# Kernel optimization log

Measured on AMD Instinct MI355X. Metric: run time of the kernel, lower is better.

The kernel has to match this reference:

```python
import jax, jax.numpy as jnp
import numpy as np

E_LAMBDA = 1e-4


def _conv1d(x, w, b=None, pad=0):
    # x: (C, L) unbatched, w: (O, I, K)
    y = jax.lax.conv_general_dilated(
        x[None], w, window_strides=(1,), padding=[(pad, pad)],
        dimension_numbers=("NCH", "OIH", "NCH"))[0]
    if b is not None:
        y = y + b[:, None]
    return y


def _avg_pool2(x):
    # kernel 2 stride 2 along last axis; x: (C, L) -> (C, L//2)
    C, L = x.shape
    return x.reshape(C, L // 2, 2).mean(axis=-1)


def _simam(x):
    # x: (C, L); torch version runs on (1, C, L) so stats are global
    n = x.shape[0] * x.shape[1] - 1
    d = (x - x.mean()) ** 2
    y = d / (4.0 * (d.sum() / n + E_LAMBDA)) + 0.5
    return x + x * jax.nn.sigmoid(y)


def setup_inputs() -> dict:
    key = jax.random.key(0)
    ks = jax.random.split(key, 6)
    C, L = 2048, 4096  # L must equal 2*C for Tiss broadcast to be valid
    inp = jax.random.normal(ks[0], (C, L), dtype=jnp.float32)
    insum = jax.random.normal(ks[1], (C, L), dtype=jnp.float32)
    conv1_w = jax.random.normal(ks[2], (C, C, 3), dtype=jnp.float32) * (1.0 / np.sqrt(3 * C))
    fc_w = jax.random.normal(ks[3], (C, C, 1), dtype=jnp.float32) * (1.0 / np.sqrt(C))
    fc_b = jax.random.normal(ks[4], (C,), dtype=jnp.float32) * 0.01
    mix_w = jnp.array([-0.8], dtype=jnp.float32)
    return {"input": inp, "insum": insum, "conv1_w": conv1_w,
            "fc_w": fc_w, "fc_b": fc_b, "mix_w": mix_w}


def reference(input, insum, conv1_w, fc_w, fc_b, mix_w):
    x = _avg_pool2(input)        # (C, L/2)
    x_mfcc = _avg_pool2(insum)   # (C, L/2)

    input_new = _simam(input)
    insum_new = _simam(insum)

    x1 = _conv1d(x, conv1_w, pad=1)          # (C, L/2)
    x_mfcc1 = _conv1d(x_mfcc, conv1_w, pad=1)
    x2 = _conv1d(x, fc_w, fc_b, pad=0).T      # (L/2, C)
    x_mfcc2 = _conv1d(x_mfcc1, fc_w, fc_b, pad=0).T  # (L/2, C)

    out1 = jax.nn.sigmoid((x1 @ x_mfcc2).sum(axis=1))          # (C,)
    out2 = jax.nn.sigmoid((x_mfcc1.T @ x2.T).sum(axis=1))      # (L/2,) == (C,)

    mf = jax.nn.sigmoid(mix_w)                                  # (1,)
    out = out1 * mf + out2 * (1.0 - mf)                         # (C,)

    out = jax.nn.sigmoid(_conv1d(out[:, None], conv1_w, pad=1))  # (C, 1)

    input_insum = input_new * 0.6 + insum_new * 0.4             # (C, L)
    return input_insum * out
```

## Files before the change

### kernel.cpp

```cpp
#include <hip/hip_runtime.h>
#include <math.h>

#define C  2048
#define L  4096
#define L2 2048
#define CW3 6144

constexpr size_t OFF_RS_A = 0;
constexpr size_t OFF_RQ_A = 2048;
constexpr size_t OFF_RS_B = 4096;
constexpr size_t OFF_RQ_B = 6144;
constexpr size_t OFF_SCAL = 8192;
constexpr size_t OFF_V    = 8208;
constexpr size_t OFF_O2   = 10256;
constexpr size_t OFF_S    = 12304;
constexpr size_t OFF_U    = 14352;
constexpr size_t OFF_MIX  = 20496;

constexpr size_t CWP_OFF = 0;
constexpr size_t GP_OFF  = 65536;
constexpr size_t HP_OFF  = 458752;

__device__ __forceinline__ float wredf(float v) {
#pragma unroll
  for (int o = 32; o; o >>= 1) v += __shfl_down(v, o, 64);
  return v;
}
__device__ __forceinline__ double wredd(double v) {
#pragma unroll
  for (int o = 32; o; o >>= 1) v += __shfl_down(v, o, 64);
  return v;
}
__device__ __forceinline__ float sigm(float x) { return 1.f / (1.f + expf(-x)); }
__device__ __forceinline__ float simam1(float x, float m, float cf) {
  float d = x - m;
  float y = d * d * cf + 0.5f;
  return x * (1.f + 1.f / (1.f + expf(-y)));
}

__global__ void k1(const float* __restrict__ A, const float* __restrict__ B,
                   const float* __restrict__ fc_w, float* __restrict__ ws,
                   float* __restrict__ scr) {
  int u = blockIdx.x, tid = threadIdx.x;
  if (u < 2048) {
    __shared__ float sm[16];
    const float4* pa = (const float4*)(A + (size_t)u * L);
    const float4* pb = (const float4*)(B + (size_t)u * L);
    float sa = 0.f, qa = 0.f, sb = 0.f, qb = 0.f;
#pragma unroll
    for (int i = tid; i < L / 4; i += 256) {
      float4 va = pa[i], vb = pb[i];
      sa += (va.x + va.y) + (va.z + va.w);
      qa += (va.x * va.x + va.y * va.y) + (va.z * va.z + va.w * va.w);
      sb += (vb.x + vb.y) + (vb.z + vb.w);
      qb += (vb.x * vb.x + vb.y * vb.y) + (vb.z * vb.z + vb.w * vb.w);
    }
    sa = wredf(sa); qa = wredf(qa); sb = wredf(sb); qb = wredf(qb);
    int lane = tid & 63, wv = tid >> 6;
    if (!lane) { sm[wv] = sa; sm[4 + wv] = qa; sm[8 + wv] = sb; sm[12 + wv] = qb; }
    __syncthreads();
    if (!tid) {
      ws[OFF_RS_A + u] = sm[0] + sm[1] + sm[2] + sm[3];
      ws[OFF_RQ_A + u] = sm[4] + sm[5] + sm[6] + sm[7];
      ws[OFF_RS_B + u] = sm[8] + sm[9] + sm[10] + sm[11];
      ws[OFF_RQ_B + u] = sm[12] + sm[13] + sm[14] + sm[15];
    }
  } else {
    int cb = u - 2048;
    int rg = cb >> 3;
    int col = (cb & 7) * 256 + tid;
    const float* p = fc_w + (size_t)rg * 64 * C + col;
    float acc = 0.f;
#pragma unroll 8
    for (int k = 0; k < 64; ++k) acc += p[(size_t)k * C];
    scr[CWP_OFF + (size_t)rg * 2048 + col] = acc;
  }
}

__global__ void k2(const float* __restrict__ fc_w, const float* __restrict__ fc_b,
                   float* __restrict__ ws) {
  int u = blockIdx.x, tid = threadIdx.x;
  int lane = tid & 63, wv = tid >> 6;
  if (u < 512) {
    __shared__ float sl[16];
    int r0 = u * 4;
    const float4* rx = (const float4*)(ws + OFF_RS_A);
    const float4* w4 = (const float4*)fc_w;
    float a0 = 0.f, a1 = 0.f, a2 = 0.f, a3 = 0.f;
#pragma unroll
    for (int i = tid; i < C / 4; i += 256) {
      float4 r = rx[i];
      float4 w0 = w4[(size_t)(r0 + 0) * 512 + i];
      float4 w1 = w4[(size_t)(r0 + 1) * 512 + i];
      float4 w2 = w4[(size_t)(r0 + 2) * 512 + i];
      float4 w3 = w4[(size_t)(r0 + 3) * 512 + i];
      a0 += w0.x * r.x + w0.y * r.y + w0.z * r.z + w0.w * r.w;
      a1 += w1.x * r.x + w1.y * r.y + w1.z * r.z + w1.w * r.w;
      a2 += w2.x * r.x + w2.y * r.y + w2.z * r.z + w2.w * r.w;
      a3 += w3.x * r.x + w3.y * r.y + w3.z * r.z + w3.w * r.w;
    }
    a0 = wredf(a0); a1 = wredf(a1); a2 = wredf(a2); a3 = wredf(a3);
    if (!lane) { sl[wv] = a0; sl[4 + wv] = a1; sl[8 + wv] = a2; sl[12 + wv] = a3; }
    __syncthreads();
    if (tid < 4) {
      float s_ = sl[tid * 4 + 0] + sl[tid * 4 + 1] + sl[tid * 4 + 2] + sl[tid * 4 + 3];
      ws[OFF_S + r0 + tid] = 0.5f * s_ + (float)L2 * fc_b[r0 + tid];
    }
  } else {
    __shared__ double sd[5];
    const float* arr = ws + (wv == 0 ? OFF_RS_A : wv == 1 ? OFF_RQ_A
                                                          : wv == 2 ? OFF_RS_B : OFF_RQ_B);
    double acc = 0.0, accb = 0.0;
    for (int i = lane; i < 2048; i += 64) {
      acc += (double)arr[i];
      if (wv == 0) accb += (double)fc_b[i];
    }
    acc = wredd(acc);
    if (wv == 0) accb = wredd(accb);
    if (!lane) { sd[wv] = acc; if (wv == 0) sd[4] = accb; }
    __syncthreads();
    if (!tid) {
      const double N = (double)C * (double)L, n = N - 1.0;
      double dA = sd[1] - sd[0] * sd[0] / N;
      double dB = sd[3] - sd[2] * sd[2] / N;
      float* sc = ws + OFF_SCAL;
      sc[0] = (float)(sd[0] / N);
      sc[1] = (float)(1.0 / (4.0 * (dA / n + 1e-4)));
      sc[2] = (float)(sd[2] / N);
      sc[3] = (float)(1.0 / (4.0 * (dB / n + 1e-4)));
      sc[4] = (float)sd[4];
    }
  }
}

__global__ void k3(const float* __restrict__ conv1_w, const float* __restrict__ ws,
                   float* __restrict__ scr) {
  __shared__ float lcw[32], ls[32];
  int u = blockIdx.x, tid = threadIdx.x;
  int rg = u / 6, cc = u % 6;
  int i0 = rg * 32;
  int col4 = cc * 256 + tid;
  if (tid < 32) {
    float a = 0.f;
#pragma unroll 8
    for (int g = 0; g < 32; ++g) a += scr[CWP_OFF + (size_t)g * 2048 + i0 + tid];
    lcw[tid] = a;
    ls[tid] = ws[OFF_S + i0 + tid];
  }
  __syncthreads();
  const float4* cv = (const float4*)conv1_w;
  float4 g4 = {0.f, 0.f, 0.f, 0.f}, h4 = {0.f, 0.f, 0.f, 0.f};
#pragma unroll 8
  for (int k = 0; k < 32; ++k) {
    float4 w = cv[(size_t)(i0 + k) * 1536 + col4];
    float cwv = lcw[k], sv = ls[k];
    g4.x += cwv * w.x; g4.y += cwv * w.y; g4.z += cwv * w.z; g4.w += cwv * w.w;
    h4.x += sv * w.x;  h4.y += sv * w.y;  h4.z += sv * w.z;  h4.w += sv * w.w;
  }
  ((float4*)(scr + GP_OFF + (size_t)rg * 6144))[col4] = g4;
  ((float4*)(scr + HP_OFF + (size_t)rg * 6144))[col4] = h4;
}

__global__ void k4(const float* __restrict__ insum, const float* __restrict__ scr,
                   float* __restrict__ ws) {
  __shared__ float gs[96], hs[96];
  int u = blockIdx.x, tid = threadIdx.x;
  int kb = u & 7, cg = u >> 3;
  int c0 = cg * 32;
  int k = kb * 256 + tid;
  if (tid < 192) {
    int t = (tid < 96) ? tid : tid - 96;
    const float* base = scr + ((tid < 96) ? GP_OFF : HP_OFF) + (size_t)c0 * 3 + t;
    float a = 0.f;
#pragma unroll 8
    for (int g = 0; g < 64; ++g) a += base[(size_t)g * 6144];
    if (tid < 96) gs[t] = a; else hs[t] = a;
  }
  __syncthreads();
  float accv = 0.f, acco = 0.f;
#pragma unroll 8
  for (int c = 0; c < 32; ++c) {
    const float* row = insum + (size_t)(c0 + c) * L;
    float2 fm = *(const float2*)(row + 2 * k);
    float xc = 0.5f * (fm.x + fm.y);
    float xl = 0.f, xr = 0.f;
    if (k > 0)      { float2 f = *(const float2*)(row + 2 * k - 2); xl = 0.5f * (f.x + f.y); }
    if (k < L2 - 1) { float2 f = *(const float2*)(row + 2 * k + 2); xr = 0.5f * (f.x + f.y); }
    accv += gs[c * 3] * xl + gs[c * 3 + 1] * xc + gs[c * 3 + 2] * xr;
    acco += hs[c * 3] * xl + hs[c * 3 + 1] * xc + hs[c * 3 + 2] * xr;
  }
  atomicAdd(ws + OFF_V + k, accv);
  atomicAdd(ws + OFF_O2 + k, acco);
}

__global__ void k5(const float* __restrict__ input, float* __restrict__ ws) {
  __shared__ float vsh[2050];
  __shared__ float s12[12];
  int u = blockIdx.x, tid = threadIdx.x;
  float sb = (ws + OFF_SCAL)[4];
  if (tid == 0) { vsh[0] = 0.f; vsh[2049] = 0.f; }
  for (int j = tid; j < L2; j += 256) vsh[1 + j] = (ws + OFF_V)[j] + sb;
  __syncthreads();
  const float4* prow = (const float4*)(input + (size_t)u * L);
  float a0 = 0.f, a1 = 0.f, a2 = 0.f;
#pragma unroll
  for (int i = tid; i < L / 4; i += 256) {
    float4 f = prow[i];
    float p0 = 0.5f * (f.x + f.y), p1 = 0.5f * (f.z + f.w);
    int j = 2 * i;
    a0 += p0 * vsh[j + 2] + p1 * vsh[j + 3];
    a1 += p0 * vsh[j + 1] + p1 * vsh[j + 2];
    a2 += p0 * vsh[j]     + p1 * vsh[j + 1];
  }
  a0 = wredf(a0); a1 = wredf(a1); a2 = wredf(a2);
  int lane = tid & 63, wv = tid >> 6;
  if (!lane) { s12[wv] = a0; s12[4 + wv] = a1; s12[8 + wv] = a2; }
  __syncthreads();
  if (!tid) {
    (ws + OFF_U)[u * 3 + 0] = s12[0] + s12[1] + s12[2] + s12[3];
    (ws + OFF_U)[u * 3 + 1] = s12[4] + s12[5] + s12[6] + s12[7];
    (ws + OFF_U)[u * 3 + 2] = s12[8] + s12[9] + s12[10] + s12[11];
  }
}

__global__ void k6(const float* __restrict__ conv1_w, const float* __restrict__ mix_w,
                   float* __restrict__ ws) {
  __shared__ float sl[4];
  int u = blockIdx.x, tid = threadIdx.x;
  const float4* w4p = (const float4*)(conv1_w + (size_t)u * CW3);
  const float4* u4 = (const float4*)(ws + OFF_U);
  float acc = 0.f;
#pragma unroll
  for (int m = tid; m < CW3 / 4; m += 256) {
    float4 wv = w4p[m], uv = u4[m];
    acc += wv.x * uv.x + wv.y * uv.y + wv.z * uv.z + wv.w * uv.w;
  }
  acc = wredf(acc);
  int lane = tid & 63, wv = tid >> 6;
  if (!lane) sl[wv] = acc;
  __syncthreads();
  if (!tid) {
    float mfv = sigm(mix_w[0]);
    float o1 = sigm(sl[0] + sl[1] + sl[2] + sl[3]);
    float o2 = sigm((ws + OFF_O2)[u]);
    (ws + OFF_MIX)[u] = o1 * mfv + o2 * (1.f - mfv);
  }
}

__global__ void k7(const float* __restrict__ input, const float* __restrict__ insum,
                   const float* __restrict__ conv1_w, float* __restrict__ out,
                   const float* __restrict__ ws) {
  __shared__ float sl[4];
  __shared__ float shov;
  int u = blockIdx.x, tid = threadIdx.x;
  const float4* w4p = (const float4*)(conv1_w + (size_t)u * CW3);
  const float4* m4 = (const float4*)(ws + OFF_MIX);
  float acc = 0.f;
#pragma unroll
  for (int p = tid; p < 512; p += 256) {
    float4 f0 = w4p[3 * p], f1 = w4p[3 * p + 1], f2 = w4p[3 * p + 2];
    float4 m = m4[p];
    acc += f0.y * m.x + f1.x * m.y + f1.w * m.z + f2.z * m.w;
  }
  acc = wredf(acc);
  int lane = tid & 63, wv = tid >> 6;
  if (!lane) sl[wv] = acc;
  __syncthreads();
  if (!tid) shov = sigm(sl[0] + sl[1] + sl[2] + sl[3]);
  __syncthreads();
  float ovc = shov;
  const float* scal = ws + OFF_SCAL;
  float mA = scal[0], cA = scal[1], mB = scal[2], cB = scal[3];
  size_t base = (size_t)u * L;
  const float4* pa = (const float4*)(input + base);
  const float4* pb = (const float4*)(insum + base);
  float4* po = (float4*)(out + base);
#pragma unroll
  for (int i = tid; i < L / 4; i += 256) {
    float4 a = pa[i], b = pb[i], r;
    r.x = (simam1(a.x, mA, cA) * 0.6f + simam1(b.x, mB, cB) * 0.4f) * ovc;
    r.y = (simam1(a.y, mA, cA) * 0.6f + simam1(b.y, mB, cB) * 0.4f) * ovc;
    r.z = (simam1(a.z, mA, cA) * 0.6f + simam1(b.z, mB, cB) * 0.4f) * ovc;
    r.w = (simam1(a.w, mA, cA) * 0.6f + simam1(b.w, mB, cB) * 0.4f) * ovc;
    po[i] = r;
  }
}

extern "C" void kernel_launch(void* const* d_in, const int* in_sizes, int n_in,
                              void* d_out, int out_size, void* d_ws, size_t ws_size,
                              hipStream_t stream) {
  const float* input   = (const float*)d_in[0];
  const float* insum   = (const float*)d_in[1];
  const float* conv1_w = (const float*)d_in[2];
  const float* fc_w    = (const float*)d_in[3];
  const float* fc_b    = (const float*)d_in[4];
  const float* mix_w   = (const float*)d_in[5];
  float* out = (float*)d_out;
  float* ws  = (float*)d_ws;

  hipMemsetAsync((char*)d_ws + OFF_V * 4, 0, 4096 * 4, stream);

  dim3 b(256);
  k1<<<2304, b, 0, stream>>>(input, insum, fc_w, ws, out);
  k2<<<513, b, 0, stream>>>(fc_w, fc_b, ws);
  k3<<<384, b, 0, stream>>>(conv1_w, ws, out);
  k4<<<512, b, 0, stream>>>(insum, out, ws);
  k5<<<2048, b, 0, stream>>>(input, ws);
  k6<<<2048, b, 0, stream>>>(conv1_w, mix_w, ws);
  k7<<<2048, b, 0, stream>>>(input, insum, conv1_w, out, ws);
}
```

Before: 246.8 us.

## Fuse fc_w GEMV into conv-weight kernel, fold memset into k1, shuffle neighbors in k4

The separate k2 kernel, which computed the fc_w·rowsum GEMV and the global statistics, is merged into k3. Each of k3's 384 blocks now recomputes the 32 fc rows it needs locally, and one extra block handles the global statistics. The hipMemsetAsync of the V/O2 accumulators moves into 16 extra blocks of k1. In k4, left and right pooled neighbors now come from wave shuffles instead of extra global loads. Together these remove two launches and some redundant memory traffic, but k3 now re-reads fc_w rows 6 times (once per column chunk), which adds global traffic.

```diff
diff --git a/kernel.cpp b/kernel.cpp
--- a/kernel.cpp
+++ b/kernel.cpp
@@ -13,9 +13,8 @@
 constexpr size_t OFF_SCAL = 8192;
 constexpr size_t OFF_V    = 8208;
 constexpr size_t OFF_O2   = 10256;
-constexpr size_t OFF_S    = 12304;
-constexpr size_t OFF_U    = 14352;
-constexpr size_t OFF_MIX  = 20496;
+constexpr size_t OFF_U    = 12304;
+constexpr size_t OFF_MIX  = 18448;
 
 constexpr size_t CWP_OFF = 0;
 constexpr size_t GP_OFF  = 65536;
@@ -65,7 +64,7 @@
       ws[OFF_RS_B + u] = sm[8] + sm[9] + sm[10] + sm[11];
       ws[OFF_RQ_B + u] = sm[12] + sm[13] + sm[14] + sm[15];
     }
-  } else {
+  } else if (u < 2304) {
     int cb = u - 2048;
     int rg = cb >> 3;
     int col = (cb & 7) * 256 + tid;
@@ -74,40 +73,57 @@
 #pragma unroll 8
     for (int k = 0; k < 64; ++k) acc += p[(size_t)k * C];
     scr[CWP_OFF + (size_t)rg * 2048 + col] = acc;
-  }
-}
-
-__global__ void k2(const float* __restrict__ fc_w, const float* __restrict__ fc_b,
-                   float* __restrict__ ws) {
-  int u = blockIdx.x, tid = threadIdx.x;
-  int lane = tid & 63, wv = tid >> 6;
-  if (u < 512) {
-    __shared__ float sl[16];
-    int r0 = u * 4;
-    const float4* rx = (const float4*)(ws + OFF_RS_A);
-    const float4* w4 = (const float4*)fc_w;
-    float a0 = 0.f, a1 = 0.f, a2 = 0.f, a3 = 0.f;
-#pragma unroll
-    for (int i = tid; i < C / 4; i += 256) {
-      float4 r = rx[i];
-      float4 w0 = w4[(size_t)(r0 + 0) * 512 + i];
-      float4 w1 = w4[(size_t)(r0 + 1) * 512 + i];
-      float4 w2 = w4[(size_t)(r0 + 2) * 512 + i];
-      float4 w3 = w4[(size_t)(r0 + 3) * 512 + i];
-      a0 += w0.x * r.x + w0.y * r.y + w0.z * r.z + w0.w * r.w;
-      a1 += w1.x * r.x + w1.y * r.y + w1.z * r.z + w1.w * r.w;
-      a2 += w2.x * r.x + w2.y * r.y + w2.z * r.z + w2.w * r.w;
-      a3 += w3.x * r.x + w3.y * r.y + w3.z * r.z + w3.w * r.w;
-    }
-    a0 = wredf(a0); a1 = wredf(a1); a2 = wredf(a2); a3 = wredf(a3);
-    if (!lane) { sl[wv] = a0; sl[4 + wv] = a1; sl[8 + wv] = a2; sl[12 + wv] = a3; }
+  } else {
+    int idx = (u - 2304) * 256 + tid;
+    ws[OFF_V + idx] = 0.f;
+  }
+}
+
+__global__ void k3(const float* __restrict__ conv1_w, const float* __restrict__ fc_w,
+                   const float* __restrict__ fc_b, float* __restrict__ ws,
+                   float* __restrict__ scr) {
+  int u = blockIdx.x, tid = threadIdx.x;
+  if (u < 384) {
+    __shared__ float lcw[32], ls[32];
+    int rg = u / 6, cc = u % 6;
+    int i0 = rg * 32;
+    int col4 = cc * 256 + tid;
+    {
+      int r = tid >> 3, g = tid & 7;
+      const float4* wrow = (const float4*)(fc_w + (size_t)(i0 + r) * C);
+      const float4* rx = (const float4*)(ws + OFF_RS_A);
+      float acc = 0.f;
+#pragma unroll 8
+      for (int j = g; j < C / 4; j += 8) {
+        float4 w = wrow[j], rv = rx[j];
+        acc += w.x * rv.x + w.y * rv.y + w.z * rv.z + w.w * rv.w;
+      }
+      acc += __shfl_xor(acc, 1, 64);
+      acc += __shfl_xor(acc, 2, 64);
+      acc += __shfl_xor(acc, 4, 64);
+      if (g == 0) ls[r] = 0.5f * acc + (float)L2 * fc_b[i0 + r];
+    }
+    if (tid < 32) {
+      float a = 0.f;
+#pragma unroll 8
+      for (int g = 0; g < 32; ++g) a += scr[CWP_OFF + (size_t)g * 2048 + i0 + tid];
+      lcw[tid] = a;
+    }
     __syncthreads();
-    if (tid < 4) {
-      float s_ = sl[tid * 4 + 0] + sl[tid * 4 + 1] + sl[tid * 4 + 2] + sl[tid * 4 + 3];
-      ws[OFF_S + r0 + tid] = 0.5f * s_ + (float)L2 * fc_b[r0 + tid];
-    }
+    const float4* cv = (const float4*)conv1_w;
+    float4 g4 = {0.f, 0.f, 0.f, 0.f}, h4 = {0.f, 0.f, 0.f, 0.f};
+#pragma unroll 8
+    for (int k = 0; k < 32; ++k) {
+      float4 w = cv[(size_t)(i0 + k) * 1536 + col4];
+      float cwv = lcw[k], sv = ls[k];
+      g4.x += cwv * w.x; g4.y += cwv * w.y; g4.z += cwv * w.z; g4.w += cwv * w.w;
+      h4.x += sv * w.x;  h4.y += sv * w.y;  h4.z += sv * w.z;  h4.w += sv * w.w;
+    }
+    ((float4*)(scr + GP_OFF + (size_t)rg * 6144))[col4] = g4;
+    ((float4*)(scr + HP_OFF + (size_t)rg * 6144))[col4] = h4;
   } else {
     __shared__ double sd[5];
+    int lane = tid & 63, wv = tid >> 6;
     const float* arr = ws + (wv == 0 ? OFF_RS_A : wv == 1 ? OFF_RQ_A
                                                           : wv == 2 ? OFF_RS_B : OFF_RQ_B);
     double acc = 0.0, accb = 0.0;
@@ -133,34 +149,6 @@
   }
 }
 
-__global__ void k3(const float* __restrict__ conv1_w, const float* __restrict__ ws,
-                   float* __restrict__ scr) {
-  __shared__ float lcw[32], ls[32];
-  int u = blockIdx.x, tid = threadIdx.x;
-  int rg = u / 6, cc = u % 6;
-  int i0 = rg * 32;
-  int col4 = cc * 256 + tid;
-  if (tid < 32) {
-    float a = 0.f;
-#pragma unroll 8
-    for (int g = 0; g < 32; ++g) a += scr[CWP_OFF + (size_t)g * 2048 + i0 + tid];
-    lcw[tid] = a;
-    ls[tid] = ws[OFF_S + i0 + tid];
-  }
-  __syncthreads();
-  const float4* cv = (const float4*)conv1_w;
-  float4 g4 = {0.f, 0.f, 0.f, 0.f}, h4 = {0.f, 0.f, 0.f, 0.f};
-#pragma unroll 8
-  for (int k = 0; k < 32; ++k) {
-    float4 w = cv[(size_t)(i0 + k) * 1536 + col4];
-    float cwv = lcw[k], sv = ls[k];
-    g4.x += cwv * w.x; g4.y += cwv * w.y; g4.z += cwv * w.z; g4.w += cwv * w.w;
-    h4.x += sv * w.x;  h4.y += sv * w.y;  h4.z += sv * w.z;  h4.w += sv * w.w;
-  }
-  ((float4*)(scr + GP_OFF + (size_t)rg * 6144))[col4] = g4;
-  ((float4*)(scr + HP_OFF + (size_t)rg * 6144))[col4] = h4;
-}
-
 __global__ void k4(const float* __restrict__ insum, const float* __restrict__ scr,
                    float* __restrict__ ws) {
   __shared__ float gs[96], hs[96];
@@ -168,6 +156,7 @@
   int kb = u & 7, cg = u >> 3;
   int c0 = cg * 32;
   int k = kb * 256 + tid;
+  int lane = tid & 63;
   if (tid < 192) {
     int t = (tid < 96) ? tid : tid - 96;
     const float* base = scr + ((tid < 96) ? GP_OFF : HP_OFF) + (size_t)c0 * 3 + t;
@@ -178,14 +167,21 @@
   }
   __syncthreads();
   float accv = 0.f, acco = 0.f;
-#pragma unroll 8
+#pragma unroll 4
   for (int c = 0; c < 32; ++c) {
     const float* row = insum + (size_t)(c0 + c) * L;
     float2 fm = *(const float2*)(row + 2 * k);
     float xc = 0.5f * (fm.x + fm.y);
-    float xl = 0.f, xr = 0.f;
-    if (k > 0)      { float2 f = *(const float2*)(row + 2 * k - 2); xl = 0.5f * (f.x + f.y); }
-    if (k < L2 - 1) { float2 f = *(const float2*)(row + 2 * k + 2); xr = 0.5f * (f.x + f.y); }
+    float xl = __shfl_up(xc, 1, 64);
+    float xr = __shfl_down(xc, 1, 64);
+    if (lane == 0) {
+      xl = 0.f;
+      if (k > 0) { float2 f = *(const float2*)(row + 2 * k - 2); xl = 0.5f * (f.x + f.y); }
+    }
+    if (lane == 63) {
+      xr = 0.f;
+      if (k < L2 - 1) { float2 f = *(const float2*)(row + 2 * k + 2); xr = 0.5f * (f.x + f.y); }
+    }
     accv += gs[c * 3] * xl + gs[c * 3 + 1] * xc + gs[c * 3 + 2] * xr;
     acco += hs[c * 3] * xl + hs[c * 3 + 1] * xc + hs[c * 3 + 2] * xr;
   }
@@ -298,12 +294,9 @@
   float* out = (float*)d_out;
   float* ws  = (float*)d_ws;
 
-  hipMemsetAsync((char*)d_ws + OFF_V * 4, 0, 4096 * 4, stream);
-
   dim3 b(256);
-  k1<<<2304, b, 0, stream>>>(input, insum, fc_w, ws, out);
-  k2<<<513, b, 0, stream>>>(fc_w, fc_b, ws);
-  k3<<<384, b, 0, stream>>>(conv1_w, ws, out);
+  k1<<<2320, b, 0, stream>>>(input, insum, fc_w, ws, out);
+  k3<<<385, b, 0, stream>>>(conv1_w, fc_w, fc_b, ws, out);
   k4<<<512, b, 0, stream>>>(insum, out, ws);
   k5<<<2048, b, 0, stream>>>(input, ws);
   k6<<<2048, b, 0, stream>>>(conv1_w, mix_w, ws);
```

New measurement: 252.9 us. +2.5%, slower.
